# Performance work log

Hardware: AMD Instinct MI355X
Metric: run time of the kernel (lower is better)

## Reference

```python
import jax, jax.numpy as jnp
import numpy as np

LEAKY_SLOPE = 0.2


def _sample_ball(key, n, dim, radius):
    # uniform in unit ball: normalize gaussian, scale by U^(1/dim)
    k1, k2 = jax.random.split(key)
    g = jax.random.normal(k1, (n, dim), dtype=jnp.float32)
    g = g / jnp.linalg.norm(g, axis=-1, keepdims=True)
    r = jax.random.uniform(k2, (n, 1), dtype=jnp.float32) ** (1.0 / dim)
    return radius * g * r


def setup_inputs() -> dict:
    key = jax.random.key(0)
    ks = jax.random.split(key, 8)
    B, N, D, K = 16, 4096, 3, 4096
    IN, H1, H2, OUT = K + K * D, 1024, 512, 256
    point_cloud = jax.random.normal(ks[0], (B, N, D), dtype=jnp.float32) * 0.3
    basis = _sample_ball(ks[1], K, D, 1.0)
    s = 0.02
    W1 = jax.random.normal(ks[2], (IN, H1), dtype=jnp.float32) * s
    b1 = jnp.zeros((H1,), dtype=jnp.float32)
    W2 = jax.random.normal(ks[3], (H1, H2), dtype=jnp.float32) * s
    b2 = jnp.zeros((H2,), dtype=jnp.float32)
    W3 = jax.random.normal(ks[4], (H2, OUT), dtype=jnp.float32) * s
    b3 = jnp.zeros((OUT,), dtype=jnp.float32)
    return {"point_cloud": point_cloud, "basis": basis,
            "W1": W1, "b1": b1, "W2": W2, "b2": b2, "W3": W3, "b3": b3}


def _bps_encode(pc, basis):
    # pc: [B,N,3], basis: [K,3]
    # squared cdist via gemm expansion (avoids [B,K,N,3] broadcast)
    pn = jnp.sum(pc * pc, axis=-1)                     # [B,N]
    bn = jnp.sum(basis * basis, axis=-1)               # [K]
    cross = jnp.einsum('kd,bnd->bkn', basis, pc)       # [B,K,N]
    d2 = bn[None, :, None] + pn[:, None, :] - 2.0 * cross
    idx = jnp.argmin(d2, axis=-1)                      # [B,K]
    nearest = jnp.take_along_axis(pc, idx[..., None], axis=1)  # [B,K,3]
    deltas = nearest - basis[None, :, :]               # [B,K,3]
    dists = jnp.linalg.norm(deltas, axis=-1)           # [B,K]
    return dists, deltas


def reference(point_cloud, basis, W1, b1, W2, b2, W3, b3):
    B = point_cloud.shape[0]
    dists, deltas = _bps_encode(point_cloud, basis)
    bps_feature = jnp.concatenate([dists, deltas.reshape(B, -1)], axis=-1)  # [B, K+3K]
    h = bps_feature @ W1 + b1
    h = jnp.where(h >= 0, h, LEAKY_SLOPE * h)
    h = h @ W2 + b2
    h = jnp.where(h >= 0, h, LEAKY_SLOPE * h)
    global_feature = h @ W3 + b3
    return (global_feature, bps_feature[:, None, :])
```

## Files before the change

kernel.cpp:

```cpp
#include <hip/hip_runtime.h>

#define LEAKY_SLOPE 0.2f

constexpr int B_   = 16;
constexpr int N_   = 4096;
constexpr int K_   = 4096;
constexpr int IN_  = 16384;
constexpr int H1_  = 1024;
constexpr int H2_  = 512;
constexpr int OUT_ = 256;

constexpr int NCH = 64;
constexpr int NPC = N_ / NCH;
constexpr int KPT = 8;
constexpr int KTB = 256 * KPT;

__global__ __launch_bounds__(256) void enc_partial(
    const float* __restrict__ pc, const float* __restrict__ basis,
    unsigned long long* __restrict__ chunkmin)
{
#pragma clang fp contract(off)
    __shared__ float4 pts[NPC + 1];
    const int kt = blockIdx.x;
    const int b  = blockIdx.y;
    const int c  = blockIdx.z;
    const int n0 = c * NPC;

    if (threadIdx.x < NPC) {
        const float* pp = pc + ((size_t)b * N_ + n0 + threadIdx.x) * 3;
        float x = pp[0], y = pp[1], z = pp[2];
        pts[threadIdx.x] = make_float4(x, y, z, (x * x + y * y) + z * z);
    }
    if (threadIdx.x == 0) pts[NPC] = make_float4(0.f, 0.f, 0.f, 0.f);
    __syncthreads();

    const int k0 = kt * KTB + (int)threadIdx.x;
    float nbx[KPT], nby[KPT], nbz[KPT], best[KPT];
    int   bi[KPT];
#pragma unroll
    for (int q = 0; q < KPT; ++q) {
        int k = k0 + q * 256;
        nbx[q] = -2.0f * basis[k * 3 + 0];
        nby[q] = -2.0f * basis[k * 3 + 1];
        nbz[q] = -2.0f * basis[k * 3 + 2];
        best[q] = 3.4028235e38f;
        bi[q] = 0;
    }

    float4 pcur = pts[0];
#pragma unroll 4
    for (int n = 0; n < NPC; ++n) {
        float4 pnext = pts[n + 1];
#pragma unroll
        for (int q = 0; q < KPT; ++q) {
            float e2 = __builtin_fmaf(nbx[q], pcur.x,
                        __builtin_fmaf(nby[q], pcur.y,
                         __builtin_fmaf(nbz[q], pcur.z, pcur.w)));
            if (e2 < best[q]) { best[q] = e2; bi[q] = n0 + n; }
        }
        pcur = pnext;
    }

    unsigned long long* dst = chunkmin + ((size_t)(c * B_ + b)) * K_;
#pragma unroll
    for (int q = 0; q < KPT; ++q) {
        unsigned u = __float_as_uint(best[q]);
        u = (u & 0x80000000u) ? ~u : (u | 0x80000000u);
        dst[k0 + q * 256] =
            ((unsigned long long)u << 32) | (unsigned)bi[q];
    }
}

__global__ __launch_bounds__(256) void enc_reduce_finish(
    const float* __restrict__ pc, const float* __restrict__ basis,
    const unsigned long long* __restrict__ chunkmin,
    float* __restrict__ bps_out)
{
#pragma clang fp contract(off)
    const int t = blockIdx.x * 256 + (int)threadIdx.x;
    const int b = t >> 12;
    const int k = t & (K_ - 1);

    unsigned long long vmin = 0xFFFFFFFFFFFFFFFFull;
#pragma unroll 8
    for (int c = 0; c < NCH; ++c) {
        unsigned long long v = chunkmin[((size_t)(c * B_ + b)) * K_ + k];
        vmin = (v < vmin) ? v : vmin;
    }
    const int bi = (int)(unsigned)(vmin & 0xffffffffull);

    const float* p = pc + ((size_t)b * N_ + bi) * 3;
    float dx = p[0] - basis[k * 3 + 0];
    float dy = p[1] - basis[k * 3 + 1];
    float dz = p[2] - basis[k * 3 + 2];
    float dist = sqrtf((dx * dx + dy * dy) + dz * dz);

    float* row = bps_out + (size_t)b * IN_;
    row[k]              = dist;
    row[K_ + 3 * k + 0] = dx;
    row[K_ + 3 * k + 1] = dy;
    row[K_ + 3 * k + 2] = dz;
}

template<int ILEN, int NCOLS>
__global__ __launch_bounds__(256) void gemm1(
    const float* __restrict__ A, const float* __restrict__ W,
    float* __restrict__ part)
{
    __shared__ float red[4][64][33];
    const int lane = (int)threadIdx.x & 63;
    const int w    = __builtin_amdgcn_readfirstlane((int)threadIdx.x >> 6);
    const int j0   = blockIdx.x * 128 + lane * 2;
    const int i0   = blockIdx.y * ILEN + w * (ILEN / 4);

    float2 acc[16];
#pragma unroll
    for (int r = 0; r < 16; ++r) acc[r] = make_float2(0.f, 0.f);

#pragma unroll 4
    for (int i = i0; i < i0 + ILEN / 4; ++i) {
        float2 wv = *(const float2*)(W + (size_t)i * NCOLS + j0);
#pragma unroll
        for (int r = 0; r < 16; ++r) {
            float a = A[(size_t)r * IN_ + i];
            acc[r].x = __builtin_fmaf(a, wv.x, acc[r].x);
            acc[r].y = __builtin_fmaf(a, wv.y, acc[r].y);
        }
    }

#pragma unroll
    for (int r = 0; r < 16; ++r) {
        red[w][lane][2 * r]     = acc[r].x;
        red[w][lane][2 * r + 1] = acc[r].y;
    }
    __syncthreads();

    float* base = part + (size_t)blockIdx.y * 16 * NCOLS + blockIdx.x * 128 + lane * 2;
    const int b0 = w * 4;
#pragma unroll
    for (int b = b0; b < b0 + 4; ++b) {
        float sx = 0.f, sy = 0.f;
#pragma unroll
        for (int ww = 0; ww < 4; ++ww) {
            sx += red[ww][lane][2 * b];
            sy += red[ww][lane][2 * b + 1];
        }
        *(float2*)(base + (size_t)b * NCOLS) = make_float2(sx, sy);
    }
}

__global__ __launch_bounds__(256) void reduce_act1(
    const float* __restrict__ part, const float* __restrict__ bias,
    float* __restrict__ outT)
{
    const int p = blockIdx.x * 256 + (int)threadIdx.x;
    float s = 0.0f;
#pragma unroll 8
    for (int c = 0; c < 64; ++c) s += part[(size_t)c * (16 * H1_) + p];
    const int col = p & (H1_ - 1);
    const int b   = p >> 10;
    s += bias[col];
    s = fmaxf(s, LEAKY_SLOPE * s);
    outT[(size_t)col * 16 + b] = s;
}

template<int KDIM, int NCOLS>
__global__ __launch_bounds__(256) void gemm_mid(
    const float* __restrict__ AT, const float* __restrict__ W,
    float* __restrict__ part)
{
    __shared__ float red[4][64][17];
    const int lane = (int)threadIdx.x & 63;
    const int w    = __builtin_amdgcn_readfirstlane((int)threadIdx.x >> 6);
    const int cb   = blockIdx.x;
    const int s    = blockIdx.y;
    const int j    = cb * 64 + lane;
    constexpr int KS = KDIM / 8;
    constexpr int KW = KS / 4;
    const int i0 = s * KS + w * KW;

    float acc[16];
#pragma unroll
    for (int r = 0; r < 16; ++r) acc[r] = 0.0f;

#pragma unroll 4
    for (int i = i0; i < i0 + KW; ++i) {
        float wv = W[(size_t)i * NCOLS + j];
        const float4* Ar = (const float4*)(AT + (size_t)i * 16);
        float4 q0 = Ar[0], q1 = Ar[1], q2 = Ar[2], q3 = Ar[3];
        acc[0]  = __builtin_fmaf(q0.x, wv, acc[0]);
        acc[1]  = __builtin_fmaf(q0.y, wv, acc[1]);
        acc[2]  = __builtin_fmaf(q0.z, wv, acc[2]);
        acc[3]  = __builtin_fmaf(q0.w, wv, acc[3]);
        acc[4]  = __builtin_fmaf(q1.x, wv, acc[4]);
        acc[5]  = __builtin_fmaf(q1.y, wv, acc[5]);
        acc[6]  = __builtin_fmaf(q1.z, wv, acc[6]);
        acc[7]  = __builtin_fmaf(q1.w, wv, acc[7]);
        acc[8]  = __builtin_fmaf(q2.x, wv, acc[8]);
        acc[9]  = __builtin_fmaf(q2.y, wv, acc[9]);
        acc[10] = __builtin_fmaf(q2.z, wv, acc[10]);
        acc[11] = __builtin_fmaf(q2.w, wv, acc[11]);
        acc[12] = __builtin_fmaf(q3.x, wv, acc[12]);
        acc[13] = __builtin_fmaf(q3.y, wv, acc[13]);
        acc[14] = __builtin_fmaf(q3.z, wv, acc[14]);
        acc[15] = __builtin_fmaf(q3.w, wv, acc[15]);
    }

#pragma unroll
    for (int r = 0; r < 16; ++r) red[w][lane][r] = acc[r];
    __syncthreads();

#pragma unroll
    for (int q = 0; q < 4; ++q) {
        int p  = (int)threadIdx.x * 4 + q;
        int cl = p >> 4;
        int bt = p & 15;
        float ssum = 0.0f;
#pragma unroll
        for (int ww = 0; ww < 4; ++ww) ssum += red[ww][cl][bt];
        part[((size_t)s * NCOLS + cb * 64 + cl) * 16 + bt] = ssum;
    }
}

template<int KDIM, int NCOLS>
__global__ __launch_bounds__(256) void gemm_last(
    const float* __restrict__ h2part, const float* __restrict__ b2,
    const float* __restrict__ W, float* __restrict__ part)
{
    __shared__ float aT[64][20];
    __shared__ float red[4][64][17];
    const int lane = (int)threadIdx.x & 63;
    const int w    = __builtin_amdgcn_readfirstlane((int)threadIdx.x >> 6);
    const int cb   = blockIdx.x;
    const int s    = blockIdx.y;
    constexpr int KS = KDIM / 8;

    {
        const int il  = (int)threadIdx.x >> 2;
        const int btq = ((int)threadIdx.x & 3) * 4;
        const int i   = s * KS + il;
        float4 sum = make_float4(0.f, 0.f, 0.f, 0.f);
#pragma unroll
        for (int sl = 0; sl < 8; ++sl) {
            const float4 v = *(const float4*)(h2part +
                ((size_t)sl * H2_ + i) * 16 + btq);
            sum.x += v.x; sum.y += v.y; sum.z += v.z; sum.w += v.w;
        }
        const float bb = b2[i];
        sum.x += bb; sum.y += bb; sum.z += bb; sum.w += bb;
        sum.x = fmaxf(sum.x, LEAKY_SLOPE * sum.x);
        sum.y = fmaxf(sum.y, LEAKY_SLOPE * sum.y);
        sum.z = fmaxf(sum.z, LEAKY_SLOPE * sum.z);
        sum.w = fmaxf(sum.w, LEAKY_SLOPE * sum.w);
        *(float4*)&aT[il][btq] = sum;
    }
    __syncthreads();

    const int j  = cb * 64 + lane;
    const int i0 = w * 16;
    float acc[16];
#pragma unroll
    for (int r = 0; r < 16; ++r) acc[r] = 0.0f;

#pragma unroll 4
    for (int il = i0; il < i0 + 16; ++il) {
        float wv = W[((size_t)(s * KS + il)) * NCOLS + j];
        float4 q0 = *(const float4*)&aT[il][0];
        float4 q1 = *(const float4*)&aT[il][4];
        float4 q2 = *(const float4*)&aT[il][8];
        float4 q3 = *(const float4*)&aT[il][12];
        acc[0]  = __builtin_fmaf(q0.x, wv, acc[0]);
        acc[1]  = __builtin_fmaf(q0.y, wv, acc[1]);
        acc[2]  = __builtin_fmaf(q0.z, wv, acc[2]);
        acc[3]  = __builtin_fmaf(q0.w, wv, acc[3]);
        acc[4]  = __builtin_fmaf(q1.x, wv, acc[4]);
        acc[5]  = __builtin_fmaf(q1.y, wv, acc[5]);
        acc[6]  = __builtin_fmaf(q1.z, wv, acc[6]);
        acc[7]  = __builtin_fmaf(q1.w, wv, acc[7]);
        acc[8]  = __builtin_fmaf(q2.x, wv, acc[8]);
        acc[9]  = __builtin_fmaf(q2.y, wv, acc[9]);
        acc[10] = __builtin_fmaf(q2.z, wv, acc[10]);
        acc[11] = __builtin_fmaf(q2.w, wv, acc[11]);
        acc[12] = __builtin_fmaf(q3.x, wv, acc[12]);
        acc[13] = __builtin_fmaf(q3.y, wv, acc[13]);
        acc[14] = __builtin_fmaf(q3.z, wv, acc[14]);
        acc[15] = __builtin_fmaf(q3.w, wv, acc[15]);
    }

#pragma unroll
    for (int r = 0; r < 16; ++r) red[w][lane][r] = acc[r];
    __syncthreads();

#pragma unroll
    for (int q = 0; q < 4; ++q) {
        int p  = (int)threadIdx.x * 4 + q;
        int cl = p >> 4;
        int bt = p & 15;
        float ssum = 0.0f;
#pragma unroll
        for (int ww = 0; ww < 4; ++ww) ssum += red[ww][cl][bt];
        part[((size_t)s * NCOLS + cb * 64 + cl) * 16 + bt] = ssum;
    }
}

__global__ __launch_bounds__(256) void out_final(
    const float* __restrict__ h3part, const float* __restrict__ b3,
    float* __restrict__ out)
{
    const int t   = blockIdx.x * 256 + (int)threadIdx.x;
    const int col = t >> 4;
    const int bt  = t & 15;
    float s = b3[col];
#pragma unroll
    for (int sl = 0; sl < 8; ++sl)
        s += h3part[((size_t)sl * OUT_ + col) * 16 + bt];
    out[(size_t)bt * OUT_ + col] = s;
}

extern "C" void kernel_launch(void* const* d_in, const int* in_sizes, int n_in,
                              void* d_out, int out_size, void* d_ws, size_t ws_size,
                              hipStream_t stream)
{
    const float* pc    = (const float*)d_in[0];
    const float* basis = (const float*)d_in[1];
    const float* W1    = (const float*)d_in[2];
    const float* b1    = (const float*)d_in[3];
    const float* W2    = (const float*)d_in[4];
    const float* b2    = (const float*)d_in[5];
    const float* W3    = (const float*)d_in[6];
    const float* b3    = (const float*)d_in[7];

    float* out   = (float*)d_out;
    float* gfeat = out;
    float* bps   = out + B_ * OUT_;

    char* ws = (char*)d_ws;
    unsigned long long* chunkmin = (unsigned long long*)ws;
    float* partial = (float*)(ws + (size_t)32 * 1024 * 1024);
    float* h1T     = (float*)(ws + (size_t)36 * 1024 * 1024);
    float* h2part  = (float*)(ws + (size_t)36 * 1024 * 1024 + 64 * 1024);
    float* h3part  = (float*)(ws + (size_t)36 * 1024 * 1024 + 320 * 1024);

    enc_partial<<<dim3(K_ / KTB, B_, NCH), 256, 0, stream>>>(pc, basis, chunkmin);
    enc_reduce_finish<<<(B_ * K_) / 256, 256, 0, stream>>>(pc, basis, chunkmin, bps);
    gemm1<256, H1_><<<dim3(8, 64), 256, 0, stream>>>(bps, W1, partial);
    reduce_act1<<<(H1_ * 16) / 256, 256, 0, stream>>>(partial, b1, h1T);
    gemm_mid<1024, H2_><<<dim3(8, 8), 256, 0, stream>>>(h1T, W2, h2part);
    gemm_last<512, OUT_><<<dim3(4, 8), 256, 0, stream>>>(h2part, b2, W3, h3part);
    out_final<<<16, 256, 0, stream>>>(h3part, b3, gfeat);
}
```

Measured before the change: 178.4 us.

## Pack encoder FMAs into float2 vectors and fuse layer-1 reduction into gemm_mid

The nearest-point search now computes two basis points at once with 2-wide vector FMAs, aiming at packed FP32 math on CDNA. The separate reduce_act1 kernel is removed. gemm1 now writes its partials in a transposed [col][batch] layout, and gemm_mid sums the 64 split-K partials, adds bias and applies leaky ReLU into shared memory before its GEMM. This drops one launch and one global round trip, but each of the 8 column blocks re-reduces the same partial slices, which is redundant reads.

Result: slower. 187.5 us (+5.1%).

```diff
diff --git a/kernel.cpp b/kernel.cpp
--- a/kernel.cpp
+++ b/kernel.cpp
@@ -1,6 +1,8 @@
 #include <hip/hip_runtime.h>
 
 #define LEAKY_SLOPE 0.2f
+
+typedef float f32x2 __attribute__((ext_vector_type(2)));
 
 constexpr int B_   = 16;
 constexpr int N_   = 4096;
@@ -35,28 +37,35 @@
     __syncthreads();
 
     const int k0 = kt * KTB + (int)threadIdx.x;
-    float nbx[KPT], nby[KPT], nbz[KPT], best[KPT];
+    f32x2 nbx[4], nby[4], nbz[4];
+    float best[KPT];
     int   bi[KPT];
 #pragma unroll
-    for (int q = 0; q < KPT; ++q) {
-        int k = k0 + q * 256;
-        nbx[q] = -2.0f * basis[k * 3 + 0];
-        nby[q] = -2.0f * basis[k * 3 + 1];
-        nbz[q] = -2.0f * basis[k * 3 + 2];
-        best[q] = 3.4028235e38f;
-        bi[q] = 0;
-    }
+    for (int h = 0; h < 4; ++h) {
+        int ka = k0 + (2 * h) * 256;
+        int kb = ka + 256;
+        nbx[h] = (f32x2){ -2.0f * basis[ka * 3 + 0], -2.0f * basis[kb * 3 + 0] };
+        nby[h] = (f32x2){ -2.0f * basis[ka * 3 + 1], -2.0f * basis[kb * 3 + 1] };
+        nbz[h] = (f32x2){ -2.0f * basis[ka * 3 + 2], -2.0f * basis[kb * 3 + 2] };
+    }
+#pragma unroll
+    for (int q = 0; q < KPT; ++q) { best[q] = 3.4028235e38f; bi[q] = 0; }
 
     float4 pcur = pts[0];
 #pragma unroll 4
     for (int n = 0; n < NPC; ++n) {
         float4 pnext = pts[n + 1];
-#pragma unroll
-        for (int q = 0; q < KPT; ++q) {
-            float e2 = __builtin_fmaf(nbx[q], pcur.x,
-                        __builtin_fmaf(nby[q], pcur.y,
-                         __builtin_fmaf(nbz[q], pcur.z, pcur.w)));
-            if (e2 < best[q]) { best[q] = e2; bi[q] = n0 + n; }
+        const f32x2 px = { pcur.x, pcur.x };
+        const f32x2 py = { pcur.y, pcur.y };
+        const f32x2 pz = { pcur.z, pcur.z };
+        const f32x2 pw = { pcur.w, pcur.w };
+#pragma unroll
+        for (int h = 0; h < 4; ++h) {
+            f32x2 e2 = __builtin_elementwise_fma(nbx[h], px,
+                        __builtin_elementwise_fma(nby[h], py,
+                         __builtin_elementwise_fma(nbz[h], pz, pw)));
+            if (e2.x < best[2 * h])     { best[2 * h]     = e2.x; bi[2 * h]     = n0 + n; }
+            if (e2.y < best[2 * h + 1]) { best[2 * h + 1] = e2.y; bi[2 * h + 1] = n0 + n; }
         }
         pcur = pnext;
     }
@@ -135,59 +144,73 @@
     }
     __syncthreads();
 
-    float* base = part + (size_t)blockIdx.y * 16 * NCOLS + blockIdx.x * 128 + lane * 2;
-    const int b0 = w * 4;
-#pragma unroll
-    for (int b = b0; b < b0 + 4; ++b) {
-        float sx = 0.f, sy = 0.f;
-#pragma unroll
-        for (int ww = 0; ww < 4; ++ww) {
-            sx += red[ww][lane][2 * b];
-            sy += red[ww][lane][2 * b + 1];
-        }
-        *(float2*)(base + (size_t)b * NCOLS) = make_float2(sx, sy);
-    }
-}
-
-__global__ __launch_bounds__(256) void reduce_act1(
-    const float* __restrict__ part, const float* __restrict__ bias,
-    float* __restrict__ outT)
-{
-    const int p = blockIdx.x * 256 + (int)threadIdx.x;
-    float s = 0.0f;
-#pragma unroll 8
-    for (int c = 0; c < 64; ++c) s += part[(size_t)c * (16 * H1_) + p];
-    const int col = p & (H1_ - 1);
-    const int b   = p >> 10;
-    s += bias[col];
-    s = fmaxf(s, LEAKY_SLOPE * s);
-    outT[(size_t)col * 16 + b] = s;
+    {
+        const int t   = (int)threadIdx.x;
+        const int l   = t >> 2;
+        const int par = (t >> 1) & 1;
+        const int bh  = (t & 1) * 8;
+        float vv[8];
+#pragma unroll
+        for (int b = 0; b < 8; ++b) {
+            float s = 0.f;
+#pragma unroll
+            for (int ww = 0; ww < 4; ++ww) s += red[ww][l][2 * (bh + b) + par];
+            vv[b] = s;
+        }
+        float* dst = part + ((size_t)blockIdx.y * NCOLS
+                             + blockIdx.x * 128 + 2 * l + par) * 16 + bh;
+        *(float4*)(dst)     = make_float4(vv[0], vv[1], vv[2], vv[3]);
+        *(float4*)(dst + 4) = make_float4(vv[4], vv[5], vv[6], vv[7]);
+    }
 }
 
 template<int KDIM, int NCOLS>
 __global__ __launch_bounds__(256) void gemm_mid(
-    const float* __restrict__ AT, const float* __restrict__ W,
-    float* __restrict__ part)
-{
+    const float* __restrict__ part1, const float* __restrict__ b1,
+    const float* __restrict__ W, float* __restrict__ part)
+{
+    __shared__ float aT[128][16];
     __shared__ float red[4][64][17];
     const int lane = (int)threadIdx.x & 63;
     const int w    = __builtin_amdgcn_readfirstlane((int)threadIdx.x >> 6);
     const int cb   = blockIdx.x;
     const int s    = blockIdx.y;
-    const int j    = cb * 64 + lane;
     constexpr int KS = KDIM / 8;
-    constexpr int KW = KS / 4;
-    const int i0 = s * KS + w * KW;
-
+
+#pragma unroll
+    for (int u = 0; u < 2; ++u) {
+        const int item = (int)threadIdx.x * 2 + u;
+        const int il   = item >> 2;
+        const int btq  = (item & 3) * 4;
+        float4 acc4 = make_float4(0.f, 0.f, 0.f, 0.f);
+        for (int c = 0; c < 64; ++c) {
+            const float4 v = *(const float4*)(part1 +
+                ((size_t)c * H1_ + s * KS + il) * 16 + btq);
+            acc4.x += v.x; acc4.y += v.y; acc4.z += v.z; acc4.w += v.w;
+        }
+        const float bb = b1[s * KS + il];
+        acc4.x += bb; acc4.y += bb; acc4.z += bb; acc4.w += bb;
+        acc4.x = fmaxf(acc4.x, LEAKY_SLOPE * acc4.x);
+        acc4.y = fmaxf(acc4.y, LEAKY_SLOPE * acc4.y);
+        acc4.z = fmaxf(acc4.z, LEAKY_SLOPE * acc4.z);
+        acc4.w = fmaxf(acc4.w, LEAKY_SLOPE * acc4.w);
+        *(float4*)&aT[il][btq] = acc4;
+    }
+    __syncthreads();
+
+    const int j  = cb * 64 + lane;
+    const int i0 = w * 32;
     float acc[16];
 #pragma unroll
     for (int r = 0; r < 16; ++r) acc[r] = 0.0f;
 
 #pragma unroll 4
-    for (int i = i0; i < i0 + KW; ++i) {
-        float wv = W[(size_t)i * NCOLS + j];
-        const float4* Ar = (const float4*)(AT + (size_t)i * 16);
-        float4 q0 = Ar[0], q1 = Ar[1], q2 = Ar[2], q3 = Ar[3];
+    for (int il = i0; il < i0 + 32; ++il) {
+        float wv = W[((size_t)(s * KS + il)) * NCOLS + j];
+        float4 q0 = *(const float4*)&aT[il][0];
+        float4 q1 = *(const float4*)&aT[il][4];
+        float4 q2 = *(const float4*)&aT[il][8];
+        float4 q3 = *(const float4*)&aT[il][12];
         acc[0]  = __builtin_fmaf(q0.x, wv, acc[0]);
         acc[1]  = __builtin_fmaf(q0.y, wv, acc[1]);
         acc[2]  = __builtin_fmaf(q0.z, wv, acc[2]);
@@ -337,15 +360,13 @@
     char* ws = (char*)d_ws;
     unsigned long long* chunkmin = (unsigned long long*)ws;
     float* partial = (float*)(ws + (size_t)32 * 1024 * 1024);
-    float* h1T     = (float*)(ws + (size_t)36 * 1024 * 1024);
-    float* h2part  = (float*)(ws + (size_t)36 * 1024 * 1024 + 64 * 1024);
-    float* h3part  = (float*)(ws + (size_t)36 * 1024 * 1024 + 320 * 1024);
+    float* h2part  = (float*)(ws + (size_t)36 * 1024 * 1024);
+    float* h3part  = (float*)(ws + (size_t)36 * 1024 * 1024 + 256 * 1024);
 
     enc_partial<<<dim3(K_ / KTB, B_, NCH), 256, 0, stream>>>(pc, basis, chunkmin);
     enc_reduce_finish<<<(B_ * K_) / 256, 256, 0, stream>>>(pc, basis, chunkmin, bps);
     gemm1<256, H1_><<<dim3(8, 64), 256, 0, stream>>>(bps, W1, partial);
-    reduce_act1<<<(H1_ * 16) / 256, 256, 0, stream>>>(partial, b1, h1T);
-    gemm_mid<1024, H2_><<<dim3(8, 8), 256, 0, stream>>>(h1T, W2, h2part);
+    gemm_mid<1024, H2_><<<dim3(8, 8), 256, 0, stream>>>(partial, b1, W2, h2part);
     gemm_last<512, OUT_><<<dim3(4, 8), 256, 0, stream>>>(h2part, b2, W3, h3part);
     out_final<<<16, 256, 0, stream>>>(h3part, b3, gfeat);
 }
```

## Track only min distance per chunk, recover argmin by rescanning winning chunk

Applied to the files above, without the earlier changes.

The partial-encoding kernel now keeps only the per-chunk minimum distance with fminf instead of carrying the index through a compare-and-select, and writes 4-byte floats instead of packed 64-bit keys. The reduce kernel picks the winning chunk and rescans its 64 points to recover the nearest point. This cuts the inner-loop instruction count and halves the intermediate traffic, at the cost of an extra 64-point scan per output and possible tie-breaking differences from the reference argmin.

Measured after the change: 170.9 us. 4.2% less time.

```diff
diff --git a/kernel.cpp b/kernel.cpp
--- a/kernel.cpp
+++ b/kernel.cpp
@@ -17,7 +17,7 @@
 
 __global__ __launch_bounds__(256) void enc_partial(
     const float* __restrict__ pc, const float* __restrict__ basis,
-    unsigned long long* __restrict__ chunkmin)
+    float* __restrict__ chunkminf)
 {
 #pragma clang fp contract(off)
     __shared__ float4 pts[NPC + 1];
@@ -36,7 +36,6 @@
 
     const int k0 = kt * KTB + (int)threadIdx.x;
     float nbx[KPT], nby[KPT], nbz[KPT], best[KPT];
-    int   bi[KPT];
 #pragma unroll
     for (int q = 0; q < KPT; ++q) {
         int k = k0 + q * 256;
@@ -44,7 +43,6 @@
         nby[q] = -2.0f * basis[k * 3 + 1];
         nbz[q] = -2.0f * basis[k * 3 + 2];
         best[q] = 3.4028235e38f;
-        bi[q] = 0;
     }
 
     float4 pcur = pts[0];
@@ -56,24 +54,20 @@
             float e2 = __builtin_fmaf(nbx[q], pcur.x,
                         __builtin_fmaf(nby[q], pcur.y,
                          __builtin_fmaf(nbz[q], pcur.z, pcur.w)));
-            if (e2 < best[q]) { best[q] = e2; bi[q] = n0 + n; }
+            best[q] = __builtin_fminf(best[q], e2);
         }
         pcur = pnext;
     }
 
-    unsigned long long* dst = chunkmin + ((size_t)(c * B_ + b)) * K_;
-#pragma unroll
-    for (int q = 0; q < KPT; ++q) {
-        unsigned u = __float_as_uint(best[q]);
-        u = (u & 0x80000000u) ? ~u : (u | 0x80000000u);
-        dst[k0 + q * 256] =
-            ((unsigned long long)u << 32) | (unsigned)bi[q];
-    }
+    float* dst = chunkminf + ((size_t)(c * B_ + b)) * K_;
+#pragma unroll
+    for (int q = 0; q < KPT; ++q)
+        dst[k0 + q * 256] = best[q];
 }
 
 __global__ __launch_bounds__(256) void enc_reduce_finish(
     const float* __restrict__ pc, const float* __restrict__ basis,
-    const unsigned long long* __restrict__ chunkmin,
+    const float* __restrict__ chunkminf,
     float* __restrict__ bps_out)
 {
 #pragma clang fp contract(off)
@@ -81,18 +75,46 @@
     const int b = t >> 12;
     const int k = t & (K_ - 1);
 
-    unsigned long long vmin = 0xFFFFFFFFFFFFFFFFull;
+    float m = 3.4028235e38f;
+    int   cb = 0;
 #pragma unroll 8
     for (int c = 0; c < NCH; ++c) {
-        unsigned long long v = chunkmin[((size_t)(c * B_ + b)) * K_ + k];
-        vmin = (v < vmin) ? v : vmin;
-    }
-    const int bi = (int)(unsigned)(vmin & 0xffffffffull);
-
-    const float* p = pc + ((size_t)b * N_ + bi) * 3;
-    float dx = p[0] - basis[k * 3 + 0];
-    float dy = p[1] - basis[k * 3 + 1];
-    float dz = p[2] - basis[k * 3 + 2];
+        float v = chunkminf[((size_t)(c * B_ + b)) * K_ + k];
+        if (v < m) { m = v; cb = c; }
+    }
+
+    const float bx0 = basis[k * 3 + 0];
+    const float by0 = basis[k * 3 + 1];
+    const float bz0 = basis[k * 3 + 2];
+    const float nbx = -2.0f * bx0;
+    const float nby = -2.0f * by0;
+    const float nbz = -2.0f * bz0;
+
+    const float4* pch = (const float4*)(pc + ((size_t)b * N_ + cb * NPC) * 3);
+    float mm = 3.4028235e38f;
+    float px = 0.f, py = 0.f, pz = 0.f;
+#pragma unroll 4
+    for (int g = 0; g < NPC / 4; ++g) {
+        float4 q0 = pch[3 * g + 0];
+        float4 q1 = pch[3 * g + 1];
+        float4 q2 = pch[3 * g + 2];
+        float xs[4] = { q0.x, q0.w, q1.z, q2.y };
+        float ys[4] = { q0.y, q1.x, q1.w, q2.z };
+        float zs[4] = { q0.z, q1.y, q2.x, q2.w };
+#pragma unroll
+        for (int j = 0; j < 4; ++j) {
+            float x = xs[j], y = ys[j], z = zs[j];
+            float pw = (x * x + y * y) + z * z;
+            float e2 = __builtin_fmaf(nbx, x,
+                        __builtin_fmaf(nby, y,
+                         __builtin_fmaf(nbz, z, pw)));
+            if (e2 < mm) { mm = e2; px = x; py = y; pz = z; }
+        }
+    }
+
+    float dx = px - bx0;
+    float dy = py - by0;
+    float dz = pz - bz0;
     float dist = sqrtf((dx * dx + dy * dy) + dz * dz);
 
     float* row = bps_out + (size_t)b * IN_;
@@ -335,14 +357,14 @@
     float* bps   = out + B_ * OUT_;
 
     char* ws = (char*)d_ws;
-    unsigned long long* chunkmin = (unsigned long long*)ws;
-    float* partial = (float*)(ws + (size_t)32 * 1024 * 1024);
-    float* h1T     = (float*)(ws + (size_t)36 * 1024 * 1024);
-    float* h2part  = (float*)(ws + (size_t)36 * 1024 * 1024 + 64 * 1024);
-    float* h3part  = (float*)(ws + (size_t)36 * 1024 * 1024 + 320 * 1024);
-
-    enc_partial<<<dim3(K_ / KTB, B_, NCH), 256, 0, stream>>>(pc, basis, chunkmin);
-    enc_reduce_finish<<<(B_ * K_) / 256, 256, 0, stream>>>(pc, basis, chunkmin, bps);
+    float* chunkminf = (float*)ws;
+    float* partial = (float*)(ws + (size_t)16 * 1024 * 1024);
+    float* h1T     = (float*)(ws + (size_t)20 * 1024 * 1024);
+    float* h2part  = (float*)(ws + (size_t)20 * 1024 * 1024 + 64 * 1024);
+    float* h3part  = (float*)(ws + (size_t)20 * 1024 * 1024 + 320 * 1024);
+
+    enc_partial<<<dim3(K_ / KTB, B_, NCH), 256, 0, stream>>>(pc, basis, chunkminf);
+    enc_reduce_finish<<<(B_ * K_) / 256, 256, 0, stream>>>(pc, basis, chunkminf, bps);
     gemm1<256, H1_><<<dim3(8, 64), 256, 0, stream>>>(bps, W1, partial);
     reduce_act1<<<(H1_ * 16) / 256, 256, 0, stream>>>(partial, b1, h1T);
     gemm_mid<1024, H2_><<<dim3(8, 8), 256, 0, stream>>>(h1T, W2, h2part);
```
